# Kernel optimization log

Hardware: AMD Instinct MI355X
Metric: run time of the kernel (lower is better)

Reference implementation:

```python
import jax, jax.numpy as jnp
import numpy as np

N_BINS = 20  # matches ECELoss(n_bins=20) default
N, C = 1_000_000, 128


def setup_inputs() -> dict:
    key = jax.random.key(0)
    k1, k2 = jax.random.split(key)
    # module expects pre-softmaxed probabilities (logits=False path)
    logits = jax.random.normal(k1, (N, C), dtype=jnp.float32)
    outputs = jax.nn.softmax(logits, axis=1)
    labels = jax.random.randint(k2, (N,), 0, C, dtype=jnp.int32)
    return {"outputs": outputs, "labels": labels}


def reference(outputs, labels):
    # confidences, predictions = max over classes
    conf = jnp.max(outputs, axis=1)          # [N]
    pred = jnp.argmax(outputs, axis=1)       # [N]
    acc = (pred == labels).astype(outputs.dtype)  # [N]

    # Equal-width bins with (lower, upper] membership, identical to
    # conf.gt(lower) & conf.le(upper) on linspace(0,1,n_bins+1) edges:
    # bin index = ceil(conf * n_bins) - 1, clipped into range.
    bin_idx = jnp.clip(jnp.ceil(conf * N_BINS).astype(jnp.int32) - 1, 0, N_BINS - 1)

    sum_conf = jax.ops.segment_sum(conf, bin_idx, num_segments=N_BINS)  # [n_bins]
    sum_acc = jax.ops.segment_sum(acc, bin_idx, num_segments=N_BINS)    # [n_bins]

    # |avg_conf_b - acc_b| * (count_b / N) == |sum_conf_b - sum_acc_b| / N,
    # and empty bins contribute exactly 0 (matches the prop_in_bin>0 guard).
    n = jnp.asarray(conf.shape[0], dtype=outputs.dtype)
    ece = jnp.sum(jnp.abs(sum_conf - sum_acc)) / n
    return ece.reshape(1)  # torch version returns a shape-(1,) tensor
```

## Files before the change

### kernel.cpp

```cpp
#include <hip/hip_runtime.h>
#include <float.h>

#define N_BINS 20
#define C 128
#define NVAL (2 * N_BINS)

typedef float f32x4 __attribute__((ext_vector_type(4)));

__global__ void ece_init(float* __restrict__ slots, int total) {
    int t = blockIdx.x * blockDim.x + threadIdx.x;
    if (t < total) slots[t] = 0.0f;
}

__global__ __launch_bounds__(256) void ece_main(const float* __restrict__ outs,
                                                const int* __restrict__ labels,
                                                float* __restrict__ slots,
                                                int n_rows, int n_waves,
                                                int S, int priv) {
    __shared__ float s_hist[NVAL];

    const int tid = threadIdx.x;
    if (tid < NVAL) s_hist[tid] = 0.0f;
    __syncthreads();

    const int lane = tid & 63;
    const int sub  = lane & 7;
    const int rsub = lane >> 3;
    const int gwave = blockIdx.x * 4 + (tid >> 6);

    const f32x4* __restrict__ outs4 = reinterpret_cast<const f32x4*>(outs);

    for (int rowBase = gwave * 8; rowBase < n_rows; rowBase += n_waves * 8) {
        const int row = rowBase + rsub;
        const bool live = (row < n_rows);

        int   lab = -1;
        float bestVal = -FLT_MAX;
        int   bestIdx = 0x7fffffff;

        if (live) {
            if (sub == 0) lab = labels[row];
            const f32x4* p = outs4 + (size_t)row * (C / 4) + sub;
            f32x4 v[4];
            #pragma unroll
            for (int j = 0; j < 4; ++j) v[j] = p[j * 8];

            const int b0 = 4 * sub;
            bestVal = v[0].x; bestIdx = b0;
            #pragma unroll
            for (int j = 0; j < 4; ++j) {
                const int b = b0 + 32 * j;
                if (j > 0 && v[j].x > bestVal) { bestVal = v[j].x; bestIdx = b; }
                if (v[j].y > bestVal) { bestVal = v[j].y; bestIdx = b + 1; }
                if (v[j].z > bestVal) { bestVal = v[j].z; bestIdx = b + 2; }
                if (v[j].w > bestVal) { bestVal = v[j].w; bestIdx = b + 3; }
            }
        }

        #pragma unroll
        for (int m = 1; m <= 4; m <<= 1) {
            const float ov = __shfl_xor(bestVal, m);
            const int   oi = __shfl_xor(bestIdx, m);
            if (ov > bestVal || (ov == bestVal && oi < bestIdx)) {
                bestVal = ov;
                bestIdx = oi;
            }
        }

        if (sub == 0 && live) {
            int bin = (int)ceilf(bestVal * (float)N_BINS) - 1;
            bin = min(max(bin, 0), N_BINS - 1);
            atomicAdd(&s_hist[bin], bestVal);
            atomicAdd(&s_hist[N_BINS + bin], (bestIdx == lab) ? 1.0f : 0.0f);
        }
    }

    __syncthreads();
    if (tid < NVAL) {
        const int slot = blockIdx.x % S;
        if (priv) slots[(size_t)tid * S + slot] = s_hist[tid];
        else      atomicAdd(&slots[(size_t)tid * S + slot], s_hist[tid]);
    }
}

__global__ __launch_bounds__(1024) void ece_final(const float* __restrict__ slots,
                                                  float* __restrict__ out,
                                                  int S, float inv_n) {
    __shared__ float red[NVAL][16];
    __shared__ float tot[NVAL];

    const int tid = threadIdx.x;
    const int j = tid >> 4;
    const int c = tid & 15;

    if (j < NVAL) {
        const float* base = slots + (size_t)j * S;
        float p0 = 0.f, p1 = 0.f, p2 = 0.f, p3 = 0.f;
        int s = c;
        for (; s + 48 < S; s += 64) {
            p0 += base[s];
            p1 += base[s + 16];
            p2 += base[s + 32];
            p3 += base[s + 48];
        }
        for (; s < S; s += 16) p0 += base[s];
        red[j][c] = (p0 + p1) + (p2 + p3);
    }
    __syncthreads();

    if (tid < NVAL) {
        float t2 = 0.f;
        #pragma unroll
        for (int k = 0; k < 16; ++k) t2 += red[tid][k];
        tot[tid] = t2;
    }
    __syncthreads();

    if (tid < 64) {
        float d = (tid < N_BINS) ? fabsf(tot[tid] - tot[tid + N_BINS]) : 0.0f;
        #pragma unroll
        for (int m = 1; m <= 32; m <<= 1) d += __shfl_xor(d, m);
        if (tid == 0) out[0] = d * inv_n;
    }
}

extern "C" void kernel_launch(void* const* d_in, const int* in_sizes, int n_in,
                              void* d_out, int out_size, void* d_ws, size_t ws_size,
                              hipStream_t stream) {
    const float* outs   = (const float*)d_in[0];
    const int*   labels = (const int*)d_in[1];
    float*       out    = (float*)d_out;
    float*       slots  = (float*)d_ws;

    const int n_rows = in_sizes[1];
    const int blocks  = 1954;
    const int n_waves = blocks * 4;

    int S, priv;
    if (ws_size >= (size_t)blocks * NVAL * sizeof(float)) {
        S = blocks; priv = 1;
    } else {
        priv = 0;
        S = 1;
        while ((size_t)(S * 2) * NVAL * sizeof(float) <= ws_size && S * 2 < blocks)
            S <<= 1;
    }

    if (!priv) {
        const int total = S * NVAL;
        hipLaunchKernelGGL(ece_init, dim3((total + 255) / 256), dim3(256), 0,
                           stream, slots, total);
    }
    hipLaunchKernelGGL(ece_main, dim3(blocks), dim3(256), 0, stream,
                       outs, labels, slots, n_rows, n_waves, S, priv);
    hipLaunchKernelGGL(ece_final, dim3(1), dim3(1024), 0, stream,
                       slots, out, S, 1.0f / (float)n_rows);
}
```

Baseline: 106.0 us.

## Fuse final reduction into main kernel via last-block atomic counter

Result: slower. 281.9 us (+166.0%).

```diff
diff --git a/kernel.cpp b/kernel.cpp
--- a/kernel.cpp
+++ b/kernel.cpp
@@ -4,20 +4,22 @@
 #define N_BINS 20
 #define C 128
 #define NVAL (2 * N_BINS)
+#define S_SLOTS 64
+#define SLOT_FLOATS (NVAL * S_SLOTS)
 
 typedef float f32x4 __attribute__((ext_vector_type(4)));
-
-__global__ void ece_init(float* __restrict__ slots, int total) {
-    int t = blockIdx.x * blockDim.x + threadIdx.x;
-    if (t < total) slots[t] = 0.0f;
-}
 
 __global__ __launch_bounds__(256) void ece_main(const float* __restrict__ outs,
                                                 const int* __restrict__ labels,
                                                 float* __restrict__ slots,
+                                                unsigned int* __restrict__ counter,
+                                                float* __restrict__ out,
                                                 int n_rows, int n_waves,
-                                                int S, int priv) {
+                                                int nblocks, float inv_n) {
     __shared__ float s_hist[NVAL];
+    __shared__ float s_red[SLOT_FLOATS];
+    __shared__ float s_tot[NVAL];
+    __shared__ int   s_last;
 
     const int tid = threadIdx.x;
     if (tid < NVAL) s_hist[tid] = 0.0f;
@@ -76,51 +78,42 @@
     }
 
     __syncthreads();
+
     if (tid < NVAL) {
-        const int slot = blockIdx.x % S;
-        if (priv) slots[(size_t)tid * S + slot] = s_hist[tid];
-        else      atomicAdd(&slots[(size_t)tid * S + slot], s_hist[tid]);
-    }
-}
-
-__global__ __launch_bounds__(1024) void ece_final(const float* __restrict__ slots,
-                                                  float* __restrict__ out,
-                                                  int S, float inv_n) {
-    __shared__ float red[NVAL][16];
-    __shared__ float tot[NVAL];
-
-    const int tid = threadIdx.x;
-    const int j = tid >> 4;
-    const int c = tid & 15;
-
-    if (j < NVAL) {
-        const float* base = slots + (size_t)j * S;
-        float p0 = 0.f, p1 = 0.f, p2 = 0.f, p3 = 0.f;
-        int s = c;
-        for (; s + 48 < S; s += 64) {
-            p0 += base[s];
-            p1 += base[s + 16];
-            p2 += base[s + 32];
-            p3 += base[s + 48];
-        }
-        for (; s < S; s += 16) p0 += base[s];
-        red[j][c] = (p0 + p1) + (p2 + p3);
+        atomicAdd(&slots[tid * S_SLOTS + (blockIdx.x & (S_SLOTS - 1))],
+                  s_hist[tid]);
     }
     __syncthreads();
 
-    if (tid < NVAL) {
-        float t2 = 0.f;
-        #pragma unroll
-        for (int k = 0; k < 16; ++k) t2 += red[tid][k];
-        tot[tid] = t2;
+    if (tid == 0) {
+        __threadfence();
+        const unsigned int old = __hip_atomic_fetch_add(
+            counter, 1u, __ATOMIC_ACQ_REL, __HIP_MEMORY_SCOPE_AGENT);
+        s_last = (old == (unsigned int)(nblocks - 1)) ? 1 : 0;
     }
     __syncthreads();
 
-    if (tid < 64) {
-        float d = (tid < N_BINS) ? fabsf(tot[tid] - tot[tid + N_BINS]) : 0.0f;
-        #pragma unroll
-        for (int m = 1; m <= 32; m <<= 1) d += __shfl_xor(d, m);
-        if (tid == 0) out[0] = d * inv_n;
+    if (s_last) {
+        for (int f = tid; f < SLOT_FLOATS; f += 256)
+            s_red[f] = __hip_atomic_load(&slots[f], __ATOMIC_RELAXED,
+                                         __HIP_MEMORY_SCOPE_AGENT);
+        __syncthreads();
+
+        if (tid < NVAL) {
+            float t = 0.0f;
+            #pragma unroll
+            for (int s = 0; s < S_SLOTS; ++s) t += s_red[tid * S_SLOTS + s];
+            s_tot[tid] = t;
+        }
+        __syncthreads();
+
+        if (tid < 64) {
+            float d = (tid < N_BINS) ? fabsf(s_tot[tid] - s_tot[tid + N_BINS])
+                                     : 0.0f;
+            #pragma unroll
+            for (int m = 1; m <= 32; m <<= 1) d += __shfl_xor(d, m);
+            if (tid == 0) out[0] = d * inv_n;
+        }
     }
 }
 
@@ -131,28 +124,15 @@
     const int*   labels = (const int*)d_in[1];
     float*       out    = (float*)d_out;
     float*       slots  = (float*)d_ws;
+    unsigned int* counter = (unsigned int*)(slots + SLOT_FLOATS);
 
     const int n_rows = in_sizes[1];
     const int blocks  = 1954;
     const int n_waves = blocks * 4;
 
-    int S, priv;
-    if (ws_size >= (size_t)blocks * NVAL * sizeof(float)) {
-        S = blocks; priv = 1;
-    } else {
-        priv = 0;
-        S = 1;
-        while ((size_t)(S * 2) * NVAL * sizeof(float) <= ws_size && S * 2 < blocks)
-            S <<= 1;
-    }
+    hipMemsetAsync(d_ws, 0, (SLOT_FLOATS + 1) * sizeof(float), stream);
 
-    if (!priv) {
-        const int total = S * NVAL;
-        hipLaunchKernelGGL(ece_init, dim3((total + 255) / 256), dim3(256), 0,
-                           stream, slots, total);
-    }
     hipLaunchKernelGGL(ece_main, dim3(blocks), dim3(256), 0, stream,
-                       outs, labels, slots, n_rows, n_waves, S, priv);
-    hipLaunchKernelGGL(ece_final, dim3(1), dim3(1024), 0, stream,
-                       slots, out, S, 1.0f / (float)n_rows);
+                       outs, labels, slots, counter, out,
+                       n_rows, n_waves, blocks, 1.0f / (float)n_rows);
 }
```
